# Kernel optimization log

Hardware: AMD Instinct MI355X
Metric: run time of the kernel (lower is better)

## Reference

```python
import jax, jax.numpy as jnp
import numpy as np

NUM_LAYERS = 2


def setup_inputs() -> dict:
    key = jax.random.key(0)
    k1, k2, k3, k4 = jax.random.split(key, 4)
    N, E, D = 50000, 800000, 100
    features = jax.random.normal(k1, (N, D), dtype=jnp.float32)
    # stacked nn.Linear weights, one [D,D] per layer (no bias)
    W = jax.random.normal(k2, (NUM_LAYERS, D, D), dtype=jnp.float32) * 0.02
    src = jax.random.randint(k3, (E,), 0, N)
    dst = jax.random.randint(k4, (E,), 0, N)
    return {"features": features, "W": W, "src": src, "dst": dst}


def reference(features, W, src, dst):
    N, D = features.shape
    num_layers = W.shape[0]
    inv_lp1 = 1.0 / (num_layers + 1)

    # --- graph preprocessing (mirrors ItemConv.graph setter) ---
    # add self loops (fill_diag 1.0), then row-normalize by inverse degree
    loop = jnp.arange(N)
    src_all = jnp.concatenate([src, loop])  # message sources
    dst_all = jnp.concatenate([dst, loop])  # message destinations (rows of adj_t)
    deg = jax.ops.segment_sum(
        jnp.ones(src_all.shape, dtype=features.dtype), dst_all, num_segments=N
    )
    deg_inv = jnp.where(deg > 0, 1.0 / deg, 0.0)
    w = deg_inv[dst_all]  # per-edge weight: row-normalized, [E+N]

    # --- forward (LightGCN-style conv with linear projections) ---
    avg = features * inv_lp1
    x = features
    for i in range(num_layers):
        x = x @ W[i].T  # nn.Linear(D, D, bias=False)
        # SpMM: out[d] = sum_{e: dst=d} w_e * x[src_e]
        x = jax.ops.segment_sum(w[:, None] * x[src_all], dst_all, num_segments=N)
        # F.normalize(x): L2 along dim=-1 with eps=1e-12 (max-clamped norm)
        norm = jnp.linalg.norm(x, axis=-1, keepdims=True)
        avg = avg + (x / jnp.maximum(norm, 1e-12)) * inv_lp1
    return avg
```

## Files before the change

### kernel.cpp

```cpp
#include <hip/hip_runtime.h>

#define D 100
#define YSTRIDE 128
#define BSHIFT 7
#define BSIZE 128
#define BMASK 127
#define NBKMAX 512
#define EPB 2048
#define DCAP 4096

typedef __attribute__((ext_vector_type(8))) short bf8v;
typedef __attribute__((ext_vector_type(4))) float f4v;

__device__ inline unsigned short f2bf(float f) {
    unsigned u = __float_as_uint(f);
    return (unsigned short)((u + 0x7fffu + ((u >> 16) & 1u)) >> 16);
}
__device__ inline float bflo(unsigned v) { return __uint_as_float(v << 16); }
__device__ inline float bfhi(unsigned v) { return __uint_as_float(v & 0xffff0000u); }
__device__ inline unsigned short pk8(float a, float b) {
    return (unsigned short)(__builtin_amdgcn_cvt_pk_fp8_f32(a, b, 0, false) & 0xffff);
}
__device__ inline float up8lo(unsigned v) { return __builtin_amdgcn_cvt_f32_fp8((int)v, 0); }
__device__ inline float up8hi(unsigned v) { return __builtin_amdgcn_cvt_f32_fp8((int)v, 1); }

__device__ inline void acc8(float* acc, uint2 v, float w) {
    acc[0] = fmaf(__builtin_amdgcn_cvt_f32_fp8((int)v.x, 0), w, acc[0]);
    acc[1] = fmaf(__builtin_amdgcn_cvt_f32_fp8((int)v.x, 1), w, acc[1]);
    acc[2] = fmaf(__builtin_amdgcn_cvt_f32_fp8((int)v.x, 2), w, acc[2]);
    acc[3] = fmaf(__builtin_amdgcn_cvt_f32_fp8((int)v.x, 3), w, acc[3]);
    acc[4] = fmaf(__builtin_amdgcn_cvt_f32_fp8((int)v.y, 0), w, acc[4]);
    acc[5] = fmaf(__builtin_amdgcn_cvt_f32_fp8((int)v.y, 1), w, acc[5]);
    acc[6] = fmaf(__builtin_amdgcn_cvt_f32_fp8((int)v.y, 2), w, acc[6]);
    acc[7] = fmaf(__builtin_amdgcn_cvt_f32_fp8((int)v.y, 3), w, acc[7]);
}

__device__ inline void scan512_excl(int* a, int* t, int tid) {
    int v0 = a[2 * tid], v1 = a[2 * tid + 1];
    t[tid] = v0 + v1;
    __syncthreads();
    for (int off = 1; off < 256; off <<= 1) {
        int u = (tid >= off) ? t[tid - off] : 0;
        __syncthreads();
        t[tid] += u;
        __syncthreads();
    }
    int base = (tid ? t[tid - 1] : 0);
    a[2 * tid]     = base;
    a[2 * tid + 1] = base + v0;
    __syncthreads();
}

__global__ __launch_bounds__(256) void k_pre(const float* __restrict__ x0, const float* __restrict__ W,
                                             unsigned* __restrict__ s8, float* __restrict__ Wc,
                                             int* __restrict__ hist, const int* __restrict__ dst,
                                             int N, int E, int nbk, int packb, int ablk) {
    __shared__ int lhist[NBKMAX];
    int tid = threadIdx.x;
    int bx = blockIdx.x;

    if (bx < packb) {
        int t = bx * 256 + tid;
        if (t >= N * 32) return;
        int d = t >> 5, q = t & 31;
        unsigned p = 0u;
        if (q < D / 4) {
            float4 v = *(const float4*)(x0 + (long)d * D + q * 4);
            p = (unsigned)pk8(v.x, v.y) | ((unsigned)pk8(v.z, v.w) << 16);
        }
        s8[t] = p;
    } else if (bx < packb + ablk) {
        int blk = bx - packb;
        int base = blk * EPB;
        int count = min(EPB, E - base);
        for (int i = tid; i < NBKMAX; i += 256) lhist[i] = 0;
        __syncthreads();
        for (int i = tid; i < count; i += 256) atomicAdd(&lhist[dst[base + i] >> BSHIFT], 1);
        __syncthreads();
        for (int b = tid; b < NBKMAX; b += 256) hist[(long)blk * NBKMAX + b] = lhist[b];
    } else {
        int t = (bx - packb - ablk) * 256 + tid;
        if (t >= D * D) return;
        int i = t / D, j = t - i * D;
        const float* w2 = W + D * D + (long)i * D;
        float s = 0.f;
        for (int k = 0; k < D; k++) s += w2[k] * W[(long)k * D + j];
        Wc[t] = s;
    }
}

__global__ __launch_bounds__(256) void k_colscan_prep(const int* __restrict__ hist,
                                                      int* __restrict__ pref, int* __restrict__ bcnt,
                                                      int nebk, int nbk,
                                                      const float* __restrict__ W1,
                                                      const float* __restrict__ Wc,
                                                      unsigned short* __restrict__ P, int wtot) {
    int tid = threadIdx.x;
    if ((int)blockIdx.x < nbk) {
        int b = blockIdx.x;
        __shared__ int a[NBKMAX], t[256];
        int i0 = tid, i1 = tid + 256;
        a[i0] = (i0 < nebk) ? hist[(long)i0 * NBKMAX + b] : 0;
        a[i1] = (i1 < nebk) ? hist[(long)i1 * NBKMAX + b] : 0;
        __syncthreads();
        scan512_excl(a, t, tid);
        if (i0 < nebk) pref[(long)i0 * NBKMAX + b] = a[i0];
        if (i1 < nebk) pref[(long)i1 * NBKMAX + b] = a[i1];
        if (tid == 0) bcnt[b] = a[nebk];
    } else {
        int t2 = ((int)blockIdx.x - nbk) * 256 + tid;
        if (t2 >= wtot) return;
        int lane = t2 & 63;
        int r = t2 >> 6;
        int kt = r & 3;
        int r2 = r >> 2;
        int nt = r2 % 7;
        int l  = r2 / 7;
        const float* M = (l == 0) ? W1 : Wc;
        int ng = nt * 16 + (lane & 15);
        int k0 = kt * 32 + (lane >> 4) * 8;
        unsigned short u[8];
#pragma unroll
        for (int j = 0; j < 8; j++) {
            int k = k0 + j;
            u[j] = (ng < D && k < D) ? f2bf(M[(long)ng * D + k]) : (unsigned short)0;
        }
        uint4 o;
        o.x = (unsigned)u[0] | ((unsigned)u[1] << 16);
        o.y = (unsigned)u[2] | ((unsigned)u[3] << 16);
        o.z = (unsigned)u[4] | ((unsigned)u[5] << 16);
        o.w = (unsigned)u[6] | ((unsigned)u[7] << 16);
        *(uint4*)(P + (long)t2 * 8) = o;
    }
}

__global__ __launch_bounds__(256) void k_scanB(const int* __restrict__ bcnt,
                                               int* __restrict__ boff, int nbk, int E) {
    __shared__ int a[NBKMAX], t[256];
    int tid = threadIdx.x;
    a[tid]       = (tid < nbk) ? bcnt[tid] : 0;
    a[tid + 256] = (tid + 256 < nbk) ? bcnt[tid + 256] : 0;
    __syncthreads();
    scan512_excl(a, t, tid);
    if (tid < nbk)       boff[tid] = a[tid];
    if (tid + 256 < nbk) boff[tid + 256] = a[tid + 256];
    if (tid == 0) boff[nbk] = E;
}

__global__ __launch_bounds__(256) void k_bucketC(const int* __restrict__ src,
                                                 const int* __restrict__ dst,
                                                 const int* __restrict__ boff,
                                                 const int* __restrict__ pref,
                                                 unsigned* __restrict__ ebuf, int E, int nbk) {
    __shared__ int lhist[NBKMAX], lstart[NBKMAX], runS[NBKMAX], t[256];
    __shared__ unsigned stage[EPB];
    int tid = threadIdx.x;
    int base = blockIdx.x * EPB;
    int count = min(EPB, E - base);

    for (int i = tid; i < NBKMAX; i += 256) lhist[i] = 0;
    __syncthreads();
    for (int i = tid; i < count; i += 256) atomicAdd(&lhist[dst[base + i] >> BSHIFT], 1);
    __syncthreads();
    for (int i = tid; i < NBKMAX; i += 256) lstart[i] = lhist[i];
    __syncthreads();
    scan512_excl(lstart, t, tid);
    for (int b = tid; b < nbk; b += 256)
        runS[b] = boff[b] + pref[(long)blockIdx.x * NBKMAX + b];
    __syncthreads();
    for (int i = tid; i < NBKMAX; i += 256) lhist[i] = 0;
    __syncthreads();
    for (int i = tid; i < count; i += 256) {
        int dv = dst[base + i];
        int sv = src[base + i];
        int b = dv >> BSHIFT;
        int r = atomicAdd(&lhist[b], 1);
        stage[lstart[b] + r] = ((unsigned)(dv & BMASK) << 16) | (unsigned)sv;
    }
    __syncthreads();
    int wave = tid >> 6, lane = tid & 63;
    for (int b = wave; b < nbk; b += 4) {
        int c = lhist[b], ls = lstart[b], rs = runS[b];
        for (int j = lane; j < c; j += 64) ebuf[rs + j] = stage[ls + j];
    }
}

__global__ __launch_bounds__(256) void k_bucketD(const unsigned* __restrict__ ebuf,
                                                 const int* __restrict__ bucket_off,
                                                 int* __restrict__ col, int* __restrict__ rowptr,
                                                 int N, int nbk, int E) {
    __shared__ int lh[BSIZE], ls[BSIZE];
    __shared__ int colStage[DCAP];
    int b = blockIdx.x;
    int tid = threadIdx.x;
    int beg = bucket_off[b], end = bucket_off[b + 1];
    int cnt = end - beg;

    if (tid < BSIZE) lh[tid] = 0;
    __syncthreads();
    for (int i = tid; i < cnt; i += 256) atomicAdd(&lh[ebuf[beg + i] >> 16], 1);
    __syncthreads();
    if (tid < BSIZE) ls[tid] = lh[tid];
    __syncthreads();
    for (int off = 1; off < BSIZE; off <<= 1) {
        int v = (tid >= off && tid < BSIZE) ? ls[tid - off] : 0;
        __syncthreads();
        if (tid < BSIZE) ls[tid] += v;
        __syncthreads();
    }
    if (tid < BSIZE) ls[tid] -= lh[tid];
    __syncthreads();
    int d0 = b * BSIZE;
    if (tid < BSIZE && d0 + tid < N) rowptr[d0 + tid] = beg + ls[tid];
    if (b == nbk - 1 && tid == 0) rowptr[N] = E;
    if (tid < BSIZE) lh[tid] = 0;
    __syncthreads();
    if (cnt <= DCAP) {
        for (int i = tid; i < cnt; i += 256) {
            unsigned p = ebuf[beg + i];
            int r = p >> 16, s = (int)(p & 0xffffu);
            int k = atomicAdd(&lh[r], 1);
            colStage[ls[r] + k] = s;
        }
        __syncthreads();
        for (int i = tid; i < cnt; i += 256) col[beg + i] = colStage[i];
    } else {
        for (int i = tid; i < cnt; i += 256) {
            unsigned p = ebuf[beg + i];
            int r = p >> 16, s = (int)(p & 0xffffu);
            int k = atomicAdd(&lh[r], 1);
            col[beg + ls[r] + k] = s;
        }
    }
}

__global__ __launch_bounds__(256) void k_spmm(const unsigned short* __restrict__ g8,
                                              const int* __restrict__ rowptr,
                                              const int* __restrict__ col,
                                              const unsigned* __restrict__ self16,
                                              unsigned short* __restrict__ o8,
                                              unsigned* __restrict__ o16,
                                              int write8, int N) {
    int wave = threadIdx.x >> 6;
    int lane = threadIdx.x & 63;
    int g = lane >> 4;
    int j = lane & 15;
    int d = blockIdx.x * 4 + wave;
    if (d >= N) return;

    int b0 = __builtin_amdgcn_readfirstlane(rowptr[d]);
    int e0 = __builtin_amdgcn_readfirstlane(rowptr[d + 1]);

    float acc[8];
    if (g == 0) {
        if (self16) {
            uint4 sv = *((const uint4*)(self16 + (long)d * 64) + j);
            acc[0] = bflo(sv.x); acc[1] = bfhi(sv.x);
            acc[2] = bflo(sv.y); acc[3] = bfhi(sv.y);
            acc[4] = bflo(sv.z); acc[5] = bfhi(sv.z);
            acc[6] = bflo(sv.w); acc[7] = bfhi(sv.w);
        } else {
            uint2 sv = *(const uint2*)(g8 + (long)d * 64 + j * 4);
#pragma unroll
            for (int k = 0; k < 8; k++) acc[k] = 0.f;
            acc8(acc, sv, 1.f);
        }
    } else {
#pragma unroll
        for (int k = 0; k < 8; k++) acc[k] = 0.f;
    }

    for (int win = b0; win < e0; win += 64) {
        int m = e0 - win;
        if (m > 64) m = 64;
        int c = col[win + lane];
        int t = 0;
        for (; t + 8 <= m; t += 8) {
            int sa = __shfl(c, t + g);
            int sb = __shfl(c, t + 4 + g);
            uint2 va = *(const uint2*)(g8 + (long)sa * 64 + j * 4);
            uint2 vb = *(const uint2*)(g8 + (long)sb * 64 + j * 4);
            acc8(acc, va, 1.f);
            acc8(acc, vb, 1.f);
        }
        for (; t < m; t += 4) {
            int rem = m - t;
            int idx = t + ((g < rem) ? g : 0);
            int sa = __shfl(c, idx);
            float w = (g < rem) ? 1.f : 0.f;
            uint2 va = *(const uint2*)(g8 + (long)sa * 64 + j * 4);
            acc8(acc, va, w);
        }
    }

#pragma unroll
    for (int k = 0; k < 8; k++) {
        acc[k] += __shfl_xor(acc[k], 16);
        acc[k] += __shfl_xor(acc[k], 32);
    }

    float dinv = 1.f / (float)(e0 - b0 + 1);
    float r[8];
#pragma unroll
    for (int k = 0; k < 8; k++) r[k] = acc[k] * dinv;

    if (g == 0) {
        uint4 o;
        o.x = (unsigned)f2bf(r[0]) | ((unsigned)f2bf(r[1]) << 16);
        o.y = (unsigned)f2bf(r[2]) | ((unsigned)f2bf(r[3]) << 16);
        o.z = (unsigned)f2bf(r[4]) | ((unsigned)f2bf(r[5]) << 16);
        o.w = (unsigned)f2bf(r[6]) | ((unsigned)f2bf(r[7]) << 16);
        *((uint4*)(o16 + (long)d * 64) + j) = o;
    }
    if (write8 && g == 1) {
        uint2 p;
        p.x = (unsigned)pk8(r[0], r[1]) | ((unsigned)pk8(r[2], r[3]) << 16);
        p.y = (unsigned)pk8(r[4], r[5]) | ((unsigned)pk8(r[6], r[7]) << 16);
        *((uint2*)((unsigned*)o8 + (long)d * 32) + j) = p;
    }
}

__global__ __launch_bounds__(256) void k_epi(const unsigned short* __restrict__ u16,
                                             const unsigned short* __restrict__ v16,
                                             const unsigned short* __restrict__ P,
                                             const float* __restrict__ x0,
                                             float invlp1, float* __restrict__ out, int N) {
    int wave = threadIdx.x >> 6;
    int lane = threadIdx.x & 63;
    int quad = lane >> 4;
    int l16  = lane & 15;
    int rowbase = (blockIdx.x * 4 + wave) * 16;
    if (rowbase >= N) return;
    int arow = rowbase + l16;
    if (arow >= N) arow = N - 1;

    bf8v aU[4], aV[4];
    const unsigned short* ur = u16 + (long)arow * YSTRIDE;
    const unsigned short* vr = v16 + (long)arow * YSTRIDE;
#pragma unroll
    for (int kt = 0; kt < 4; kt++) {
        int k0 = kt * 32 + quad * 8;
        union { bf8v v; uint4 u; } a, b;
        a.u = *(const uint4*)(ur + k0);
        b.u = *(const uint4*)(vr + k0);
        aU[kt] = a.v;
        aV[kt] = b.v;
    }

    f4v accU[7], accV[7];
#pragma unroll
    for (int nt = 0; nt < 7; nt++) { accU[nt] = (f4v){0,0,0,0}; accV[nt] = (f4v){0,0,0,0}; }

    const uint4* bp = (const uint4*)P;
#pragma unroll
    for (int nt = 0; nt < 7; nt++) {
#pragma unroll
        for (int kt = 0; kt < 4; kt++) {
            union { uint4 u; bf8v v; } b1, b2;
            b1.u = bp[(nt * 4 + kt) * 64 + lane];
            b2.u = bp[(28 + nt * 4 + kt) * 64 + lane];
            accU[nt] = __builtin_amdgcn_mfma_f32_16x16x32_bf16(aU[kt], b1.v, accU[nt], 0, 0, 0);
            accV[nt] = __builtin_amdgcn_mfma_f32_16x16x32_bf16(aV[kt], b2.v, accV[nt], 0, 0, 0);
        }
    }

    float sU[4], sV[4];
#pragma unroll
    for (int i = 0; i < 4; i++) {
        float nu = 0.f, nv = 0.f;
#pragma unroll
        for (int nt = 0; nt < 7; nt++) {
            nu += accU[nt][i] * accU[nt][i];
            nv += accV[nt][i] * accV[nt][i];
        }
#pragma unroll
        for (int m = 1; m < 16; m <<= 1) {
            nu += __shfl_xor(nu, m);
            nv += __shfl_xor(nv, m);
        }
        sU[i] = invlp1 / fmaxf(sqrtf(nu), 1e-12f);
        sV[i] = invlp1 / fmaxf(sqrtf(nv), 1e-12f);
    }

#pragma unroll
    for (int nt = 0; nt < 7; nt++) {
        int cc = nt * 16 + l16;
        if (cc < D) {
#pragma unroll
            for (int i = 0; i < 4; i++) {
                int rr = rowbase + quad * 4 + i;
                if (rr < N) {
                    long idx = (long)rr * D + cc;
                    out[idx] = x0[idx] * invlp1 + accU[nt][i] * sU[i] + accV[nt][i] * sV[i];
                }
            }
        }
    }
}


extern "C" void kernel_launch(void* const* d_in, const int* in_sizes, int n_in,
                              void* d_out, int out_size, void* d_ws, size_t ws_size,
                              hipStream_t stream) {
    const float* features = (const float*)d_in[0];
    const float* W        = (const float*)d_in[1];
    const int*   src      = (const int*)d_in[2];
    const int*   dstv     = (const int*)d_in[3];

    int N = in_sizes[0] / D;
    int E = in_sizes[2];
    int L = in_sizes[1] / (D * D);
    float invlp1 = 1.f / (float)(L + 1);
    int NBK = (N + BSIZE - 1) >> BSHIFT;
    int nebk = (E + EPB - 1) / EPB;

    char*  ws  = (char*)d_ws;
    size_t off = 0;
    auto alloc = [&](size_t bytes) -> void* {
        void* p = (void*)(ws + off);
        off += (bytes + 255) & ~(size_t)255;
        return p;
    };
    unsigned*       s8     = (unsigned*)alloc((size_t)N * 32 * sizeof(unsigned));
    unsigned*       u8     = (unsigned*)alloc((size_t)N * 32 * sizeof(unsigned));
    unsigned*       u16    = (unsigned*)alloc((size_t)N * 64 * sizeof(unsigned));
    unsigned*       v16    = (unsigned*)alloc((size_t)N * 64 * sizeof(unsigned));
    float*          Wc     = (float*)alloc((size_t)D * D * sizeof(float));
    unsigned short* wpack  = (unsigned short*)alloc((size_t)2 * 7 * 4 * 64 * 8 * sizeof(unsigned short));
    unsigned*       ebuf   = (unsigned*)alloc((size_t)E * sizeof(unsigned));
    int*            colb   = (int*)alloc((size_t)E * sizeof(int));
    int*            rowptr = (int*)alloc((size_t)(N + 1) * sizeof(int));
    int*            hist   = (int*)alloc((size_t)nebk * NBKMAX * sizeof(int));
    int*            pref   = (int*)alloc((size_t)nebk * NBKMAX * sizeof(int));
    int*            bcnt   = (int*)alloc((size_t)NBKMAX * sizeof(int));
    int*            boff   = (int*)alloc((size_t)(NBKMAX + 1) * sizeof(int));

    int wtot  = 2 * 7 * 4 * 64;
    int packb = (N * 32 + 255) / 256;
    int wcb   = (D * D + 255) / 256;
    int prepb = (wtot + 255) / 256;

    k_pre<<<packb + nebk + wcb, 256, 0, stream>>>(features, W, s8, Wc, hist, dstv,
                                                  N, E, NBK, packb, nebk);
    k_colscan_prep<<<NBK + prepb, 256, 0, stream>>>(hist, pref, bcnt, nebk, NBK,
                                                    W, Wc, wpack, wtot);
    k_scanB<<<1, 256, 0, stream>>>(bcnt, boff, NBK, E);
    k_bucketC<<<nebk, 256, 0, stream>>>(src, dstv, boff, pref, ebuf, E, NBK);
    k_bucketD<<<NBK, 256, 0, stream>>>(ebuf, boff, colb, rowptr, N, NBK, E);

    int spmmblocks = (N + 3) / 4;
    k_spmm<<<spmmblocks, 256, 0, stream>>>((const unsigned short*)s8, rowptr, colb,
                                           (const unsigned*)nullptr,
                                           (unsigned short*)u8, u16, 1, N);
    k_spmm<<<spmmblocks, 256, 0, stream>>>((const unsigned short*)u8, rowptr, colb,
                                           u16, (unsigned short*)nullptr, v16, 0, N);

    int nrowtiles = (N + 15) / 16;
    int epiblocks = (nrowtiles + 3) / 4;
    k_epi<<<epiblocks, 256, 0, stream>>>((const unsigned short*)u16, (const unsigned short*)v16,
                                         wpack, features, invlp1, (float*)d_out, N);
}
```

Before: 200.5 us.

## Fuse bucket scan, CSR build with first SpMM, and second SpMM with epilogue

```diff
diff --git a/kernel.cpp b/kernel.cpp
--- a/kernel.cpp
+++ b/kernel.cpp
@@ -8,6 +8,7 @@
 #define NBKMAX 512
 #define EPB 2048
 #define DCAP 4096
+#define VSTRIDE 68
 
 typedef __attribute__((ext_vector_type(8))) short bf8v;
 typedef __attribute__((ext_vector_type(4))) float f4v;
@@ -21,8 +22,6 @@
 __device__ inline unsigned short pk8(float a, float b) {
     return (unsigned short)(__builtin_amdgcn_cvt_pk_fp8_f32(a, b, 0, false) & 0xffff);
 }
-__device__ inline float up8lo(unsigned v) { return __builtin_amdgcn_cvt_f32_fp8((int)v, 0); }
-__device__ inline float up8hi(unsigned v) { return __builtin_amdgcn_cvt_f32_fp8((int)v, 1); }
 
 __device__ inline void acc8(float* acc, uint2 v, float w) {
     acc[0] = fmaf(__builtin_amdgcn_cvt_f32_fp8((int)v.x, 0), w, acc[0]);
@@ -48,6 +47,25 @@
     int base = (tid ? t[tid - 1] : 0);
     a[2 * tid]     = base;
     a[2 * tid + 1] = base + v0;
+    __syncthreads();
+}
+
+__device__ inline void scan512_excl_512(int* a, int* t, int tid) {
+    bool act = tid < 256;
+    int v0 = 0, v1 = 0;
+    if (act) { v0 = a[2 * tid]; v1 = a[2 * tid + 1]; t[tid] = v0 + v1; }
+    __syncthreads();
+    for (int off = 1; off < 256; off <<= 1) {
+        int u = (act && tid >= off) ? t[tid - off] : 0;
+        __syncthreads();
+        if (act) t[tid] += u;
+        __syncthreads();
+    }
+    if (act) {
+        int base = (tid ? t[tid - 1] : 0);
+        a[2 * tid]     = base;
+        a[2 * tid + 1] = base + v0;
+    }
     __syncthreads();
 }
 
@@ -134,30 +152,22 @@
     }
 }
 
-__global__ __launch_bounds__(256) void k_scanB(const int* __restrict__ bcnt,
-                                               int* __restrict__ boff, int nbk, int E) {
-    __shared__ int a[NBKMAX], t[256];
-    int tid = threadIdx.x;
-    a[tid]       = (tid < nbk) ? bcnt[tid] : 0;
-    a[tid + 256] = (tid + 256 < nbk) ? bcnt[tid + 256] : 0;
-    __syncthreads();
-    scan512_excl(a, t, tid);
-    if (tid < nbk)       boff[tid] = a[tid];
-    if (tid + 256 < nbk) boff[tid + 256] = a[tid + 256];
-    if (tid == 0) boff[nbk] = E;
-}
-
 __global__ __launch_bounds__(256) void k_bucketC(const int* __restrict__ src,
                                                  const int* __restrict__ dst,
-                                                 const int* __restrict__ boff,
+                                                 const int* __restrict__ bcnt,
                                                  const int* __restrict__ pref,
                                                  unsigned* __restrict__ ebuf, int E, int nbk) {
-    __shared__ int lhist[NBKMAX], lstart[NBKMAX], runS[NBKMAX], t[256];
+    __shared__ int lhist[NBKMAX], lstart[NBKMAX], runS[NBKMAX], bscan[NBKMAX], t[256];
     __shared__ unsigned stage[EPB];
     int tid = threadIdx.x;
     int base = blockIdx.x * EPB;
     int count = min(EPB, E - base);
 
+    bscan[tid]       = (tid < nbk) ? bcnt[tid] : 0;
+    bscan[tid + 256] = (tid + 256 < nbk) ? bcnt[tid + 256] : 0;
+    __syncthreads();
+    scan512_excl(bscan, t, tid);
+
     for (int i = tid; i < NBKMAX; i += 256) lhist[i] = 0;
     __syncthreads();
     for (int i = tid; i < count; i += 256) atomicAdd(&lhist[dst[base + i] >> BSHIFT], 1);
@@ -166,7 +176,7 @@
     __syncthreads();
     scan512_excl(lstart, t, tid);
     for (int b = tid; b < nbk; b += 256)
-        runS[b] = boff[b] + pref[(long)blockIdx.x * NBKMAX + b];
+        runS[b] = bscan[b] + pref[(long)blockIdx.x * NBKMAX + b];
     __syncthreads();
     for (int i = tid; i < NBKMAX; i += 256) lhist[i] = 0;
     __syncthreads();
@@ -185,20 +195,33 @@
     }
 }
 
-__global__ __launch_bounds__(256) void k_bucketD(const unsigned* __restrict__ ebuf,
-                                                 const int* __restrict__ bucket_off,
-                                                 int* __restrict__ col, int* __restrict__ rowptr,
-                                                 int N, int nbk, int E) {
+__global__ __launch_bounds__(512) void k_bDspmm(const unsigned* __restrict__ ebuf,
+                                                const int* __restrict__ bcnt,
+                                                const unsigned short* __restrict__ g8,
+                                                int* __restrict__ col, int* __restrict__ rowptr,
+                                                unsigned* __restrict__ u8,
+                                                unsigned* __restrict__ u16,
+                                                int N, int nbk, int E) {
+    __shared__ int bscan[NBKMAX], tsc[256];
     __shared__ int lh[BSIZE], ls[BSIZE];
     __shared__ int colStage[DCAP];
     int b = blockIdx.x;
     int tid = threadIdx.x;
-    int beg = bucket_off[b], end = bucket_off[b + 1];
+
+    bscan[tid < 256 ? tid : 0] = bscan[tid < 256 ? tid : 0];
+    if (tid < 256) {
+        bscan[tid]       = (tid < nbk) ? bcnt[tid] : 0;
+        bscan[tid + 256] = (tid + 256 < nbk) ? bcnt[tid + 256] : 0;
+    }
+    __syncthreads();
+    scan512_excl_512(bscan, tsc, tid);
+    int beg = bscan[b];
+    int end = (b + 1 < NBKMAX) ? bscan[b + 1] : E;
     int cnt = end - beg;
 
     if (tid < BSIZE) lh[tid] = 0;
     __syncthreads();
-    for (int i = tid; i < cnt; i += 256) atomicAdd(&lh[ebuf[beg + i] >> 16], 1);
+    for (int i = tid; i < cnt; i += 512) atomicAdd(&lh[ebuf[beg + i] >> 16], 1);
     __syncthreads();
     if (tid < BSIZE) ls[tid] = lh[tid];
     __syncthreads();
@@ -215,134 +238,172 @@
     if (b == nbk - 1 && tid == 0) rowptr[N] = E;
     if (tid < BSIZE) lh[tid] = 0;
     __syncthreads();
-    if (cnt <= DCAP) {
-        for (int i = tid; i < cnt; i += 256) {
+    bool useL = (cnt <= DCAP);
+    if (useL) {
+        for (int i = tid; i < cnt; i += 512) {
             unsigned p = ebuf[beg + i];
             int r = p >> 16, s = (int)(p & 0xffffu);
             int k = atomicAdd(&lh[r], 1);
             colStage[ls[r] + k] = s;
         }
         __syncthreads();
-        for (int i = tid; i < cnt; i += 256) col[beg + i] = colStage[i];
+        for (int i = tid; i < cnt; i += 512) col[beg + i] = colStage[i];
     } else {
-        for (int i = tid; i < cnt; i += 256) {
+        for (int i = tid; i < cnt; i += 512) {
             unsigned p = ebuf[beg + i];
             int r = p >> 16, s = (int)(p & 0xffffu);
             int k = atomicAdd(&lh[r], 1);
             col[beg + ls[r] + k] = s;
         }
     }
-}
-
-__global__ __launch_bounds__(256) void k_spmm(const unsigned short* __restrict__ g8,
-                                              const int* __restrict__ rowptr,
-                                              const int* __restrict__ col,
-                                              const unsigned* __restrict__ self16,
-                                              unsigned short* __restrict__ o8,
-                                              unsigned* __restrict__ o16,
-                                              int write8, int N) {
-    int wave = threadIdx.x >> 6;
-    int lane = threadIdx.x & 63;
-    int g = lane >> 4;
-    int j = lane & 15;
-    int d = blockIdx.x * 4 + wave;
-    if (d >= N) return;
-
-    int b0 = __builtin_amdgcn_readfirstlane(rowptr[d]);
-    int e0 = __builtin_amdgcn_readfirstlane(rowptr[d + 1]);
-
-    float acc[8];
-    if (g == 0) {
-        if (self16) {
-            uint4 sv = *((const uint4*)(self16 + (long)d * 64) + j);
-            acc[0] = bflo(sv.x); acc[1] = bfhi(sv.x);
-            acc[2] = bflo(sv.y); acc[3] = bfhi(sv.y);
-            acc[4] = bflo(sv.z); acc[5] = bfhi(sv.z);
-            acc[6] = bflo(sv.w); acc[7] = bfhi(sv.w);
-        } else {
+    __syncthreads();
+
+    int wave = tid >> 6, lane = tid & 63, g = lane >> 4, j = lane & 15;
+    for (int i = 0; i < 16; i++) {
+        int r = wave * 16 + i;
+        int d = d0 + r;
+        if (d >= N) continue;
+        int eb = ls[r];
+        int deg = lh[r];
+
+        float acc[8];
+#pragma unroll
+        for (int k = 0; k < 8; k++) acc[k] = 0.f;
+        if (g == 0) {
             uint2 sv = *(const uint2*)(g8 + (long)d * 64 + j * 4);
-#pragma unroll
-            for (int k = 0; k < 8; k++) acc[k] = 0.f;
             acc8(acc, sv, 1.f);
         }
-    } else {
-#pragma unroll
-        for (int k = 0; k < 8; k++) acc[k] = 0.f;
-    }
-
-    for (int win = b0; win < e0; win += 64) {
-        int m = e0 - win;
-        if (m > 64) m = 64;
-        int c = col[win + lane];
-        int t = 0;
-        for (; t + 8 <= m; t += 8) {
-            int sa = __shfl(c, t + g);
-            int sb = __shfl(c, t + 4 + g);
+        int t2 = 0;
+        for (; t2 + 8 <= deg; t2 += 8) {
+            int sa = useL ? colStage[eb + t2 + g]     : col[beg + eb + t2 + g];
+            int sb = useL ? colStage[eb + t2 + 4 + g] : col[beg + eb + t2 + 4 + g];
             uint2 va = *(const uint2*)(g8 + (long)sa * 64 + j * 4);
             uint2 vb = *(const uint2*)(g8 + (long)sb * 64 + j * 4);
             acc8(acc, va, 1.f);
             acc8(acc, vb, 1.f);
         }
-        for (; t < m; t += 4) {
-            int rem = m - t;
-            int idx = t + ((g < rem) ? g : 0);
-            int sa = __shfl(c, idx);
+        for (; t2 < deg; t2 += 4) {
+            int rem = deg - t2;
+            int idx = t2 + ((g < rem) ? g : 0);
+            int sa = useL ? colStage[eb + idx] : col[beg + eb + idx];
             float w = (g < rem) ? 1.f : 0.f;
             uint2 va = *(const uint2*)(g8 + (long)sa * 64 + j * 4);
             acc8(acc, va, w);
         }
-    }
-
-#pragma unroll
-    for (int k = 0; k < 8; k++) {
-        acc[k] += __shfl_xor(acc[k], 16);
-        acc[k] += __shfl_xor(acc[k], 32);
-    }
-
-    float dinv = 1.f / (float)(e0 - b0 + 1);
-    float r[8];
-#pragma unroll
-    for (int k = 0; k < 8; k++) r[k] = acc[k] * dinv;
-
-    if (g == 0) {
-        uint4 o;
-        o.x = (unsigned)f2bf(r[0]) | ((unsigned)f2bf(r[1]) << 16);
-        o.y = (unsigned)f2bf(r[2]) | ((unsigned)f2bf(r[3]) << 16);
-        o.z = (unsigned)f2bf(r[4]) | ((unsigned)f2bf(r[5]) << 16);
-        o.w = (unsigned)f2bf(r[6]) | ((unsigned)f2bf(r[7]) << 16);
-        *((uint4*)(o16 + (long)d * 64) + j) = o;
-    }
-    if (write8 && g == 1) {
-        uint2 p;
-        p.x = (unsigned)pk8(r[0], r[1]) | ((unsigned)pk8(r[2], r[3]) << 16);
-        p.y = (unsigned)pk8(r[4], r[5]) | ((unsigned)pk8(r[6], r[7]) << 16);
-        *((uint2*)((unsigned*)o8 + (long)d * 32) + j) = p;
-    }
-}
-
-__global__ __launch_bounds__(256) void k_epi(const unsigned short* __restrict__ u16,
-                                             const unsigned short* __restrict__ v16,
-                                             const unsigned short* __restrict__ P,
-                                             const float* __restrict__ x0,
-                                             float invlp1, float* __restrict__ out, int N) {
-    int wave = threadIdx.x >> 6;
-    int lane = threadIdx.x & 63;
-    int quad = lane >> 4;
-    int l16  = lane & 15;
-    int rowbase = (blockIdx.x * 4 + wave) * 16;
+#pragma unroll
+        for (int k = 0; k < 8; k++) {
+            acc[k] += __shfl_xor(acc[k], 16);
+            acc[k] += __shfl_xor(acc[k], 32);
+        }
+        float dinv = 1.f / (float)(deg + 1);
+        float rr[8];
+#pragma unroll
+        for (int k = 0; k < 8; k++) rr[k] = acc[k] * dinv;
+        if (g == 0) {
+            uint4 o;
+            o.x = (unsigned)f2bf(rr[0]) | ((unsigned)f2bf(rr[1]) << 16);
+            o.y = (unsigned)f2bf(rr[2]) | ((unsigned)f2bf(rr[3]) << 16);
+            o.z = (unsigned)f2bf(rr[4]) | ((unsigned)f2bf(rr[5]) << 16);
+            o.w = (unsigned)f2bf(rr[6]) | ((unsigned)f2bf(rr[7]) << 16);
+            *((uint4*)(u16 + (long)d * 64) + j) = o;
+        }
+        if (g == 1) {
+            uint2 p;
+            p.x = (unsigned)pk8(rr[0], rr[1]) | ((unsigned)pk8(rr[2], rr[3]) << 16);
+            p.y = (unsigned)pk8(rr[4], rr[5]) | ((unsigned)pk8(rr[6], rr[7]) << 16);
+            *((uint2*)(u8 + (long)d * 32) + j) = p;
+        }
+    }
+}
+
+__global__ __launch_bounds__(256) void k_spmm2_epi(const unsigned short* __restrict__ u8sh,
+                                                   const int* __restrict__ rowptr,
+                                                   const int* __restrict__ col,
+                                                   const unsigned* __restrict__ u16u,
+                                                   const unsigned short* __restrict__ u16,
+                                                   const unsigned short* __restrict__ P,
+                                                   const float* __restrict__ x0,
+                                                   float invlp1, float* __restrict__ out, int N) {
+    __shared__ unsigned vstage[64 * VSTRIDE];
+    int tid = threadIdx.x;
+    int wave = tid >> 6, lane = tid & 63, g = lane >> 4, j = lane & 15;
+    int quad = lane >> 4, l16 = lane & 15;
+    int rowbase = blockIdx.x * 64 + wave * 16;
+
+    int rp = 0;
+    if (lane <= 16 && rowbase + lane <= N) rp = rowptr[min(rowbase + lane, N)];
+
+    for (int i = 0; i < 16; i++) {
+        int d = rowbase + i;
+        if (d < N) {
+            int b0 = __builtin_amdgcn_readlane(rp, i);
+            int e0 = __builtin_amdgcn_readlane(rp, i + 1);
+            float acc[8];
+            if (g == 0) {
+                uint4 sv = *((const uint4*)(u16u + (long)d * 64) + j);
+                acc[0] = bflo(sv.x); acc[1] = bfhi(sv.x);
+                acc[2] = bflo(sv.y); acc[3] = bfhi(sv.y);
+                acc[4] = bflo(sv.z); acc[5] = bfhi(sv.z);
+                acc[6] = bflo(sv.w); acc[7] = bfhi(sv.w);
+            } else {
+#pragma unroll
+                for (int k = 0; k < 8; k++) acc[k] = 0.f;
+            }
+            for (int win = b0; win < e0; win += 64) {
+                int m = e0 - win;
+                if (m > 64) m = 64;
+                int c = col[win + lane];
+                int t = 0;
+                for (; t + 8 <= m; t += 8) {
+                    int sa = __shfl(c, t + g);
+                    int sb = __shfl(c, t + 4 + g);
+                    uint2 va = *(const uint2*)(u8sh + (long)sa * 64 + j * 4);
+                    uint2 vb = *(const uint2*)(u8sh + (long)sb * 64 + j * 4);
+                    acc8(acc, va, 1.f);
+                    acc8(acc, vb, 1.f);
+                }
+                for (; t < m; t += 4) {
+                    int rem = m - t;
+                    int idx = t + ((g < rem) ? g : 0);
+                    int sa = __shfl(c, idx);
+                    float w = (g < rem) ? 1.f : 0.f;
+                    uint2 va = *(const uint2*)(u8sh + (long)sa * 64 + j * 4);
+                    acc8(acc, va, w);
+                }
+            }
+#pragma unroll
+            for (int k = 0; k < 8; k++) {
+                acc[k] += __shfl_xor(acc[k], 16);
+                acc[k] += __shfl_xor(acc[k], 32);
+            }
+            float dinv = 1.f / (float)(e0 - b0 + 1);
+            float r[8];
+#pragma unroll
+            for (int k = 0; k < 8; k++) r[k] = acc[k] * dinv;
+            if (g == 0) {
+                uint4 o;
+                o.x = (unsigned)f2bf(r[0]) | ((unsigned)f2bf(r[1]) << 16);
+                o.y = (unsigned)f2bf(r[2]) | ((unsigned)f2bf(r[3]) << 16);
+                o.z = (unsigned)f2bf(r[4]) | ((unsigned)f2bf(r[5]) << 16);
+                o.w = (unsigned)f2bf(r[6]) | ((unsigned)f2bf(r[7]) << 16);
+                *(uint4*)(vstage + (long)(wave * 16 + i) * VSTRIDE + j * 4) = o;
+            }
+        }
+    }
+    __syncthreads();
+
     if (rowbase >= N) return;
     int arow = rowbase + l16;
     if (arow >= N) arow = N - 1;
 
     bf8v aU[4], aV[4];
     const unsigned short* ur = u16 + (long)arow * YSTRIDE;
-    const unsigned short* vr = v16 + (long)arow * YSTRIDE;
+    const unsigned* vr = vstage + (long)(wave * 16 + l16) * VSTRIDE;
 #pragma unroll
     for (int kt = 0; kt < 4; kt++) {
-        int k0 = kt * 32 + quad * 8;
         union { bf8v v; uint4 u; } a, b;
-        a.u = *(const uint4*)(ur + k0);
-        b.u = *(const uint4*)(vr + k0);
+        a.u = *(const uint4*)(ur + kt * 32 + quad * 8);
+        b.u = *(const uint4*)(vr + kt * 16 + quad * 4);
         aU[kt] = a.v;
         aV[kt] = b.v;
     }
@@ -424,7 +485,6 @@
     unsigned*       s8     = (unsigned*)alloc((size_t)N * 32 * sizeof(unsigned));
     unsigned*       u8     = (unsigned*)alloc((size_t)N * 32 * sizeof(unsigned));
     unsigned*       u16    = (unsigned*)alloc((size_t)N * 64 * sizeof(unsigned));
-    unsigned*       v16    = (unsigned*)alloc((size_t)N * 64 * sizeof(unsigned));
     float*          Wc     = (float*)alloc((size_t)D * D * sizeof(float));
     unsigned short* wpack  = (unsigned short*)alloc((size_t)2 * 7 * 4 * 64 * 8 * sizeof(unsigned short));
     unsigned*       ebuf   = (unsigned*)alloc((size_t)E * sizeof(unsigned));
@@ -433,7 +493,6 @@
     int*            hist   = (int*)alloc((size_t)nebk * NBKMAX * sizeof(int));
     int*            pref   = (int*)alloc((size_t)nebk * NBKMAX * sizeof(int));
     int*            bcnt   = (int*)alloc((size_t)NBKMAX * sizeof(int));
-    int*            boff   = (int*)alloc((size_t)(NBKMAX + 1) * sizeof(int));
 
     int wtot  = 2 * 7 * 4 * 64;
     int packb = (N * 32 + 255) / 256;
@@ -444,19 +503,12 @@
                                                   N, E, NBK, packb, nebk);
     k_colscan_prep<<<NBK + prepb, 256, 0, stream>>>(hist, pref, bcnt, nebk, NBK,
                                                     W, Wc, wpack, wtot);
-    k_scanB<<<1, 256, 0, stream>>>(bcnt, boff, NBK, E);
-    k_bucketC<<<nebk, 256, 0, stream>>>(src, dstv, boff, pref, ebuf, E, NBK);
-    k_bucketD<<<NBK, 256, 0, stream>>>(ebuf, boff, colb, rowptr, N, NBK, E);
-
-    int spmmblocks = (N + 3) / 4;
-    k_spmm<<<spmmblocks, 256, 0, stream>>>((const unsigned short*)s8, rowptr, colb,
-                                           (const unsigned*)nullptr,
-                                           (unsigned short*)u8, u16, 1, N);
-    k_spmm<<<spmmblocks, 256, 0, stream>>>((const unsigned short*)u8, rowptr, colb,
-                                           u16, (unsigned short*)nullptr, v16, 0, N);
-
-    int nrowtiles = (N + 15) / 16;
-    int epiblocks = (nrowtiles + 3) / 4;
-    k_epi<<<epiblocks, 256, 0, stream>>>((const unsigned short*)u16, (const unsigned short*)v16,
-                                         wpack, features, invlp1, (float*)d_out, N);
-}
+    k_bucketC<<<nebk, 256, 0, stream>>>(src, dstv, bcnt, pref, ebuf, E, NBK);
+    k_bDspmm<<<NBK, 512, 0, stream>>>(ebuf, bcnt, (const unsigned short*)s8,
+                                      colb, rowptr, u8, u16, N, NBK, E);
+
+    int epiblocks = (N + 63) / 64;
+    k_spmm2_epi<<<epiblocks, 256, 0, stream>>>((const unsigned short*)u8, rowptr, colb,
+                                               u16, (const unsigned short*)u16,
+                                               wpack, features, invlp1, (float*)d_out, N);
+}
```

Measured after the change: 221.1 us. 10.3% more time.
